# Kernel optimization log

Measured on AMD Instinct MI355X. Metric: run time of the kernel, lower is better.

## Reference

```python
import jax, jax.numpy as jnp
import numpy as np

E, M, K, N = 32, 1024, 512, 512

def setup_inputs() -> dict:
    key = jax.random.key(0)
    k1, k2, k3 = jax.random.split(key, 3)
    A = jax.random.normal(k1, (E, M, K), dtype=jnp.float32)
    B = jax.random.normal(k2, (E, N, K), dtype=jnp.float32)
    expert_num_tokens = jax.random.randint(k3, (E,), 0, M + 1, dtype=jnp.int32)
    return {"A": A, "B": B, "expert_num_tokens": expert_num_tokens}

def reference(A, B, expert_num_tokens):
    # Per-expert GEMM: C[e] = A[e] @ B[e].T  -> [E, M, N]
    C = jnp.einsum('emk,enk->emn', A, B)
    # Rows m >= expert_num_tokens[e] are never computed/stored by the kernel;
    # zero them in the reference output.
    row_valid = jnp.arange(A.shape[1])[None, :] < expert_num_tokens[:, None]  # [E, M]
    return jnp.where(row_valid[:, :, None], C, jnp.zeros((), C.dtype))
```

## Files before the change

kernel.cpp:

```cpp
#include <hip/hip_runtime.h>
#include <hip/hip_bf16.h>

#define NE 32
#define MM 1024
#define KK 512
#define NN 512
#define BM 128
#define BN 128
#define BK 32
#define LDST (BK + 8)

typedef __attribute__((ext_vector_type(8))) short bf16x8;
typedef __attribute__((ext_vector_type(4))) short shortx4;
typedef __attribute__((ext_vector_type(4))) float floatx4;

__device__ __forceinline__ short f2bf(float f) {
  union { __hip_bfloat16 b; short s; } u;
  u.b = __float2bfloat16(f);
  return u.s;
}

extern "C" __global__ __launch_bounds__(256, 2)
void expert_gemm(const float* __restrict__ A, const float* __restrict__ B,
                 const int* __restrict__ cnts, float* __restrict__ C)
{
  const int bid = blockIdx.x;
  const int e   = bid >> 5;
  const int rem = bid & 31;
  const int mt  = rem >> 2;
  const int nt  = rem & 3;
  const int m0  = mt * BM;
  const int n0  = nt * BN;
  const int cnt = cnts[e];
  const int tid = threadIdx.x;

  float* Ce = C + ((size_t)e * MM + m0) * NN + n0;

  if (m0 >= cnt) {
    float4 z = make_float4(0.f, 0.f, 0.f, 0.f);
#pragma unroll
    for (int i = 0; i < 16; ++i) {
      int idx = i * 256 + tid;
      int r = idx >> 5;
      int c = (idx & 31) << 2;
      *(float4*)(Ce + (size_t)r * NN + c) = z;
    }
    return;
  }

  const float* Ae = A + ((size_t)e * MM + m0) * KK;
  const float* Be = B + ((size_t)e * NN + n0) * KK;

  __shared__ __align__(16) short lA[BM * LDST];
  __shared__ __align__(16) short lB[BN * LDST];

  const int wave = tid >> 6;
  const int lane = tid & 63;
  const int wm = (wave >> 1) * 64;
  const int wn = (wave & 1) * 64;
  const int fr = lane & 15;
  const int kh = lane >> 4;

  const int srow = tid >> 3;
  const int scol = (tid & 7) << 2;

  floatx4 acc[4][4] = {};

  float4 ra[4], rbv[4];
#pragma unroll
  for (int p = 0; p < 4; ++p) {
    ra[p]  = *(const float4*)(Ae + (size_t)(srow + p * 32) * KK + scol);
    rbv[p] = *(const float4*)(Be + (size_t)(srow + p * 32) * KK + scol);
  }

  for (int kt = 0; kt < KK; kt += BK) {
    __syncthreads();
#pragma unroll
    for (int p = 0; p < 4; ++p) {
      shortx4 va = { f2bf(ra[p].x),  f2bf(ra[p].y),  f2bf(ra[p].z),  f2bf(ra[p].w)  };
      shortx4 vb = { f2bf(rbv[p].x), f2bf(rbv[p].y), f2bf(rbv[p].z), f2bf(rbv[p].w) };
      *(shortx4*)(lA + (srow + p * 32) * LDST + scol) = va;
      *(shortx4*)(lB + (srow + p * 32) * LDST + scol) = vb;
    }
    __syncthreads();

    if (kt + BK < KK) {
#pragma unroll
      for (int p = 0; p < 4; ++p) {
        ra[p]  = *(const float4*)(Ae + (size_t)(srow + p * 32) * KK + kt + BK + scol);
        rbv[p] = *(const float4*)(Be + (size_t)(srow + p * 32) * KK + kt + BK + scol);
      }
    }

    bf16x8 af[4], bfv[4];
#pragma unroll
    for (int i = 0; i < 4; ++i) {
      af[i]  = *(bf16x8*)(lA + (wm + i * 16 + fr) * LDST + kh * 8);
      bfv[i] = *(bf16x8*)(lB + (wn + i * 16 + fr) * LDST + kh * 8);
    }
#pragma unroll
    for (int i = 0; i < 4; ++i)
#pragma unroll
      for (int j = 0; j < 4; ++j)
        acc[i][j] = __builtin_amdgcn_mfma_f32_16x16x32_bf16(af[i], bfv[j], acc[i][j], 0, 0, 0);
  }

  const int rb_ = (lane >> 4) * 4;
#pragma unroll
  for (int i = 0; i < 4; ++i) {
#pragma unroll
    for (int r = 0; r < 4; ++r) {
      int row = wm + i * 16 + rb_ + r;
      bool valid = (m0 + row) < cnt;
#pragma unroll
      for (int j = 0; j < 4; ++j) {
        int col = wn + j * 16 + fr;
        Ce[(size_t)row * NN + col] = valid ? acc[i][j][r] : 0.0f;
      }
    }
  }
}

extern "C" void kernel_launch(void* const* d_in, const int* in_sizes, int n_in,
                              void* d_out, int out_size, void* d_ws, size_t ws_size,
                              hipStream_t stream) {
  const float* A    = (const float*)d_in[0];
  const float* B    = (const float*)d_in[1];
  const int*   cnts = (const int*)d_in[2];
  float*       C    = (float*)d_out;

  dim3 grid(NE * (MM / BM) * (NN / BN));
  dim3 block(256);
  hipLaunchKernelGGL(expert_gemm, grid, block, 0, stream, A, B, cnts, C);
}
```

Measured before the change: 173.0 us.

## Use persistent blocks with an atomic work queue over valid tiles

Adds a single-thread prepass kernel that builds a compacted list of valid GEMM tiles followed by zero-fill row-tile items. The GEMM launches 512 persistent blocks that pull items from the list through an atomic counter, so idle blocks for empty tiles no longer occupy the grid and load balances across CUs. The serial prepass and the per-item atomics and barriers add latency, and it relies on the workspace being large enough.

```diff
diff --git a/kernel.cpp b/kernel.cpp
--- a/kernel.cpp
+++ b/kernel.cpp
@@ -9,6 +9,8 @@
 #define BN 128
 #define BK 32
 #define LDST (BK + 8)
+#define NMT (MM / BM)
+#define NNT (NN / BN)
 
 typedef __attribute__((ext_vector_type(8))) short bf16x8;
 typedef __attribute__((ext_vector_type(4))) short shortx4;
@@ -20,102 +22,128 @@
   return u.s;
 }
 
+extern "C" __global__ void prepass(const int* __restrict__ cnts,
+                                   unsigned int* __restrict__ q) {
+  if (threadIdx.x == 0 && blockIdx.x == 0) {
+    int w = 2;
+    for (int e = 0; e < NE; ++e) {
+      int vt = (cnts[e] + BM - 1) / BM;
+      for (int mt = 0; mt < vt; ++mt)
+        for (int nt = 0; nt < NNT; ++nt)
+          q[w++] = ((unsigned)e << 16) | ((unsigned)mt << 8) | (unsigned)nt;
+    }
+    for (int e = 0; e < NE; ++e) {
+      int vt = (cnts[e] + BM - 1) / BM;
+      for (int mt = vt; mt < NMT; ++mt)
+        q[w++] = 0x80000000u | ((unsigned)e << 16) | ((unsigned)mt << 8);
+    }
+    q[1] = (unsigned)(w - 2);
+    q[0] = 0u;
+  }
+}
+
 extern "C" __global__ __launch_bounds__(256, 2)
 void expert_gemm(const float* __restrict__ A, const float* __restrict__ B,
-                 const int* __restrict__ cnts, float* __restrict__ C)
+                 const int* __restrict__ cnts, float* __restrict__ C,
+                 unsigned int* __restrict__ q)
 {
-  const int bid = blockIdx.x;
-  const int e   = bid >> 5;
-  const int rem = bid & 31;
-  const int mt  = rem >> 2;
-  const int nt  = rem & 3;
-  const int m0  = mt * BM;
-  const int n0  = nt * BN;
-  const int cnt = cnts[e];
-  const int tid = threadIdx.x;
-
-  float* Ce = C + ((size_t)e * MM + m0) * NN + n0;
-
-  if (m0 >= cnt) {
-    float4 z = make_float4(0.f, 0.f, 0.f, 0.f);
-#pragma unroll
-    for (int i = 0; i < 16; ++i) {
-      int idx = i * 256 + tid;
-      int r = idx >> 5;
-      int c = (idx & 31) << 2;
-      *(float4*)(Ce + (size_t)r * NN + c) = z;
-    }
-    return;
-  }
-
-  const float* Ae = A + ((size_t)e * MM + m0) * KK;
-  const float* Be = B + ((size_t)e * NN + n0) * KK;
-
   __shared__ __align__(16) short lA[BM * LDST];
   __shared__ __align__(16) short lB[BN * LDST];
+  __shared__ unsigned int item_s;
 
+  const int tid  = threadIdx.x;
   const int wave = tid >> 6;
   const int lane = tid & 63;
   const int wm = (wave >> 1) * 64;
   const int wn = (wave & 1) * 64;
   const int fr = lane & 15;
   const int kh = lane >> 4;
-
   const int srow = tid >> 3;
   const int scol = (tid & 7) << 2;
+  const unsigned total = q[1];
 
-  floatx4 acc[4][4] = {};
+  for (;;) {
+    __syncthreads();
+    if (tid == 0) item_s = atomicAdd(&q[0], 1u);
+    __syncthreads();
+    unsigned idx = item_s;
+    if (idx >= total) break;
+    unsigned it = q[2 + idx];
+    int e  = (it >> 16) & 0xFF;
+    int mt = (it >> 8) & 0xFF;
 
-  float4 ra[4], rbv[4];
+    if (it & 0x80000000u) {
+      float* Ce = C + ((size_t)e * MM + mt * BM) * NN;
+      float4 z = make_float4(0.f, 0.f, 0.f, 0.f);
 #pragma unroll
-  for (int p = 0; p < 4; ++p) {
-    ra[p]  = *(const float4*)(Ae + (size_t)(srow + p * 32) * KK + scol);
-    rbv[p] = *(const float4*)(Be + (size_t)(srow + p * 32) * KK + scol);
-  }
+      for (int i = 0; i < 64; ++i) {
+        int fidx = i * 256 + tid;
+        int r = fidx >> 7;
+        int c = (fidx & 127) << 2;
+        *(float4*)(Ce + (size_t)r * NN + c) = z;
+      }
+      continue;
+    }
 
-  for (int kt = 0; kt < KK; kt += BK) {
-    __syncthreads();
+    int nt = it & 0xFF;
+    int m0 = mt * BM, n0 = nt * BN;
+    int cnt = cnts[e];
+    const float* Ae = A + ((size_t)e * MM + m0) * KK;
+    const float* Be = B + ((size_t)e * NN + n0) * KK;
+    float* Ce = C + ((size_t)e * MM + m0) * NN + n0;
+
+    floatx4 acc[4][4] = {};
+    float4 ra[4], rbv[4];
 #pragma unroll
     for (int p = 0; p < 4; ++p) {
-      shortx4 va = { f2bf(ra[p].x),  f2bf(ra[p].y),  f2bf(ra[p].z),  f2bf(ra[p].w)  };
-      shortx4 vb = { f2bf(rbv[p].x), f2bf(rbv[p].y), f2bf(rbv[p].z), f2bf(rbv[p].w) };
-      *(shortx4*)(lA + (srow + p * 32) * LDST + scol) = va;
-      *(shortx4*)(lB + (srow + p * 32) * LDST + scol) = vb;
+      ra[p]  = *(const float4*)(Ae + (size_t)(srow + p * 32) * KK + scol);
+      rbv[p] = *(const float4*)(Be + (size_t)(srow + p * 32) * KK + scol);
     }
-    __syncthreads();
 
-    if (kt + BK < KK) {
+    for (int kt = 0; kt < KK; kt += BK) {
+      __syncthreads();
 #pragma unroll
       for (int p = 0; p < 4; ++p) {
-        ra[p]  = *(const float4*)(Ae + (size_t)(srow + p * 32) * KK + kt + BK + scol);
-        rbv[p] = *(const float4*)(Be + (size_t)(srow + p * 32) * KK + kt + BK + scol);
+        shortx4 va = { f2bf(ra[p].x),  f2bf(ra[p].y),  f2bf(ra[p].z),  f2bf(ra[p].w)  };
+        shortx4 vb = { f2bf(rbv[p].x), f2bf(rbv[p].y), f2bf(rbv[p].z), f2bf(rbv[p].w) };
+        *(shortx4*)(lA + (srow + p * 32) * LDST + scol) = va;
+        *(shortx4*)(lB + (srow + p * 32) * LDST + scol) = vb;
       }
+      __syncthreads();
+
+      if (kt + BK < KK) {
+#pragma unroll
+        for (int p = 0; p < 4; ++p) {
+          ra[p]  = *(const float4*)(Ae + (size_t)(srow + p * 32) * KK + kt + BK + scol);
+          rbv[p] = *(const float4*)(Be + (size_t)(srow + p * 32) * KK + kt + BK + scol);
+        }
+      }
+
+      bf16x8 af[4], bfv[4];
+#pragma unroll
+      for (int i = 0; i < 4; ++i) {
+        af[i]  = *(bf16x8*)(lA + (wm + i * 16 + fr) * LDST + kh * 8);
+        bfv[i] = *(bf16x8*)(lB + (wn + i * 16 + fr) * LDST + kh * 8);
+      }
+#pragma unroll
+      for (int i = 0; i < 4; ++i)
+#pragma unroll
+        for (int j = 0; j < 4; ++j)
+          acc[i][j] = __builtin_amdgcn_mfma_f32_16x16x32_bf16(af[i], bfv[j], acc[i][j], 0, 0, 0);
     }
 
-    bf16x8 af[4], bfv[4];
+    const int rb_ = (lane >> 4) * 4;
 #pragma unroll
     for (int i = 0; i < 4; ++i) {
-      af[i]  = *(bf16x8*)(lA + (wm + i * 16 + fr) * LDST + kh * 8);
-      bfv[i] = *(bf16x8*)(lB + (wn + i * 16 + fr) * LDST + kh * 8);
-    }
 #pragma unroll
-    for (int i = 0; i < 4; ++i)
+      for (int r = 0; r < 4; ++r) {
+        int row = wm + i * 16 + rb_ + r;
+        bool valid = (m0 + row) < cnt;
 #pragma unroll
-      for (int j = 0; j < 4; ++j)
-        acc[i][j] = __builtin_amdgcn_mfma_f32_16x16x32_bf16(af[i], bfv[j], acc[i][j], 0, 0, 0);
-  }
-
-  const int rb_ = (lane >> 4) * 4;
-#pragma unroll
-  for (int i = 0; i < 4; ++i) {
-#pragma unroll
-    for (int r = 0; r < 4; ++r) {
-      int row = wm + i * 16 + rb_ + r;
-      bool valid = (m0 + row) < cnt;
-#pragma unroll
-      for (int j = 0; j < 4; ++j) {
-        int col = wn + j * 16 + fr;
-        Ce[(size_t)row * NN + col] = valid ? acc[i][j][r] : 0.0f;
+        for (int j = 0; j < 4; ++j) {
+          int col = wn + j * 16 + fr;
+          Ce[(size_t)row * NN + col] = valid ? acc[i][j][r] : 0.0f;
+        }
       }
     }
   }
@@ -128,8 +156,8 @@
   const float* B    = (const float*)d_in[1];
   const int*   cnts = (const int*)d_in[2];
   float*       C    = (float*)d_out;
+  unsigned int* q   = (unsigned int*)d_ws;
 
-  dim3 grid(NE * (MM / BM) * (NN / BN));
-  dim3 block(256);
-  hipLaunchKernelGGL(expert_gemm, grid, block, 0, stream, A, B, cnts, C);
+  hipLaunchKernelGGL(prepass, dim3(1), dim3(64), 0, stream, cnts, q);
+  hipLaunchKernelGGL(expert_gemm, dim3(512), dim3(256), 0, stream, A, B, cnts, C, q);
 }
```

After: 183.2 us. 1.06x slower.

## Compact grid to valid tiles, XOR-swizzle LDS, drop register prefetch

Applied to the files above, without the earlier changes.

Each block now scans the per-expert token counts and maps itself onto a compacted list. Valid GEMM tiles come first; after them come full-row zero-fill blocks that clear 128x512 strips. This gets rid of the scattered early-exit blocks and balances the work across the grid. The LDS padding is replaced by an XOR swizzle with 16-byte bf16x8 stores, and launch bounds rise to 4 blocks per SM. In exchange the global-load prefetch that overlapped with compute is removed, and every block pays a serial 32-iteration scan over the counts.

```diff
diff --git a/kernel.cpp b/kernel.cpp
--- a/kernel.cpp
+++ b/kernel.cpp
@@ -8,10 +8,8 @@
 #define BM 128
 #define BN 128
 #define BK 32
-#define LDST (BK + 8)
 
 typedef __attribute__((ext_vector_type(8))) short bf16x8;
-typedef __attribute__((ext_vector_type(4))) short shortx4;
 typedef __attribute__((ext_vector_type(4))) float floatx4;
 
 __device__ __forceinline__ short f2bf(float f) {
@@ -20,89 +18,100 @@
   return u.s;
 }
 
-extern "C" __global__ __launch_bounds__(256, 2)
+extern "C" __global__ __launch_bounds__(256, 4)
 void expert_gemm(const float* __restrict__ A, const float* __restrict__ B,
                  const int* __restrict__ cnts, float* __restrict__ C)
 {
-  const int bid = blockIdx.x;
-  const int e   = bid >> 5;
-  const int rem = bid & 31;
-  const int mt  = rem >> 2;
-  const int nt  = rem & 3;
-  const int m0  = mt * BM;
-  const int n0  = nt * BN;
-  const int cnt = cnts[e];
+  const int b   = blockIdx.x;
   const int tid = threadIdx.x;
 
-  float* Ce = C + ((size_t)e * MM + m0) * NN + n0;
-
-  if (m0 >= cnt) {
-    float4 z = make_float4(0.f, 0.f, 0.f, 0.f);
+  int e = -1, mt = 0, nt = 0;
+  int acc = 0;
+#pragma unroll 1
+  for (int i = 0; i < NE; ++i) {
+    int vt = (cnts[i] + BM - 1) >> 7;
+    int c4 = vt << 2;
+    if (e < 0 && b < acc + c4) { int r = b - acc; e = i; mt = r >> 2; nt = r & 3; }
+    acc += c4;
+  }
+  if (e < 0) {
+    int z = b - acc, a2 = 0;
+#pragma unroll 1
+    for (int i = 0; i < NE; ++i) {
+      int vt = (cnts[i] + BM - 1) >> 7;
+      int c = 8 - vt;
+      if (e < 0 && z < a2 + c) { e = i; mt = vt + (z - a2); }
+      a2 += c;
+    }
+    if (e < 0) return;
+    float* Ce = C + ((size_t)e * MM + mt * BM) * NN;
+    float4 zf = make_float4(0.f, 0.f, 0.f, 0.f);
 #pragma unroll
-    for (int i = 0; i < 16; ++i) {
-      int idx = i * 256 + tid;
-      int r = idx >> 5;
-      int c = (idx & 31) << 2;
-      *(float4*)(Ce + (size_t)r * NN + c) = z;
+    for (int i = 0; i < 64; ++i) {
+      int fidx = i * 256 + tid;
+      int r = fidx >> 7, c = (fidx & 127) << 2;
+      *(float4*)(Ce + (size_t)r * NN + c) = zf;
     }
     return;
   }
 
+  const int m0 = mt * BM, n0 = nt * BN;
+  const int cnt = cnts[e];
   const float* Ae = A + ((size_t)e * MM + m0) * KK;
   const float* Be = B + ((size_t)e * NN + n0) * KK;
+  float* Ce = C + ((size_t)e * MM + m0) * NN + n0;
 
-  __shared__ __align__(16) short lA[BM * LDST];
-  __shared__ __align__(16) short lB[BN * LDST];
+  __shared__ __align__(16) short lA[BM * BK];
+  __shared__ __align__(16) short lB[BN * BK];
 
-  const int wave = tid >> 6;
-  const int lane = tid & 63;
-  const int wm = (wave >> 1) * 64;
-  const int wn = (wave & 1) * 64;
-  const int fr = lane & 15;
-  const int kh = lane >> 4;
+  const int wave = tid >> 6, lane = tid & 63;
+  const int wm = (wave >> 1) * 64, wn = (wave & 1) * 64;
+  const int fr = lane & 15, kh = lane >> 4;
 
-  const int srow = tid >> 3;
-  const int scol = (tid & 7) << 2;
+  const int srow = tid >> 2;
+  const int su   = tid & 3;
 
-  floatx4 acc[4][4] = {};
-
-  float4 ra[4], rbv[4];
-#pragma unroll
-  for (int p = 0; p < 4; ++p) {
-    ra[p]  = *(const float4*)(Ae + (size_t)(srow + p * 32) * KK + scol);
-    rbv[p] = *(const float4*)(Be + (size_t)(srow + p * 32) * KK + scol);
-  }
+  floatx4 acc4[4][4] = {};
 
   for (int kt = 0; kt < KK; kt += BK) {
+    float4 a0[2], a1[2], b0[2], b1[2];
+#pragma unroll
+    for (int p = 0; p < 2; ++p) {
+      int row = srow + (p << 6);
+      int col = kt + (su << 3);
+      a0[p] = *(const float4*)(Ae + (size_t)row * KK + col);
+      a1[p] = *(const float4*)(Ae + (size_t)row * KK + col + 4);
+      b0[p] = *(const float4*)(Be + (size_t)row * KK + col);
+      b1[p] = *(const float4*)(Be + (size_t)row * KK + col + 4);
+    }
+
     __syncthreads();
 #pragma unroll
-    for (int p = 0; p < 4; ++p) {
-      shortx4 va = { f2bf(ra[p].x),  f2bf(ra[p].y),  f2bf(ra[p].z),  f2bf(ra[p].w)  };
-      shortx4 vb = { f2bf(rbv[p].x), f2bf(rbv[p].y), f2bf(rbv[p].z), f2bf(rbv[p].w) };
-      *(shortx4*)(lA + (srow + p * 32) * LDST + scol) = va;
-      *(shortx4*)(lB + (srow + p * 32) * LDST + scol) = vb;
+    for (int p = 0; p < 2; ++p) {
+      int row = srow + (p << 6);
+      int unit = (row << 2) + (su ^ (row & 3));
+      bf16x8 va = { f2bf(a0[p].x), f2bf(a0[p].y), f2bf(a0[p].z), f2bf(a0[p].w),
+                    f2bf(a1[p].x), f2bf(a1[p].y), f2bf(a1[p].z), f2bf(a1[p].w) };
+      bf16x8 vb = { f2bf(b0[p].x), f2bf(b0[p].y), f2bf(b0[p].z), f2bf(b0[p].w),
+                    f2bf(b1[p].x), f2bf(b1[p].y), f2bf(b1[p].z), f2bf(b1[p].w) };
+      *(bf16x8*)(lA + (unit << 3)) = va;
+      *(bf16x8*)(lB + (unit << 3)) = vb;
     }
     __syncthreads();
-
-    if (kt + BK < KK) {
-#pragma unroll
-      for (int p = 0; p < 4; ++p) {
-        ra[p]  = *(const float4*)(Ae + (size_t)(srow + p * 32) * KK + kt + BK + scol);
-        rbv[p] = *(const float4*)(Be + (size_t)(srow + p * 32) * KK + kt + BK + scol);
-      }
-    }
 
     bf16x8 af[4], bfv[4];
 #pragma unroll
     for (int i = 0; i < 4; ++i) {
-      af[i]  = *(bf16x8*)(lA + (wm + i * 16 + fr) * LDST + kh * 8);
-      bfv[i] = *(bf16x8*)(lB + (wn + i * 16 + fr) * LDST + kh * 8);
+      int rA = wm + (i << 4) + fr;
+      af[i]  = *(const bf16x8*)(lA + ((((rA << 2) + (kh ^ (rA & 3)))) << 3));
+      int rB = wn + (i << 4) + fr;
+      bfv[i] = *(const bf16x8*)(lB + ((((rB << 2) + (kh ^ (rB & 3)))) << 3));
     }
 #pragma unroll
     for (int i = 0; i < 4; ++i)
 #pragma unroll
       for (int j = 0; j < 4; ++j)
-        acc[i][j] = __builtin_amdgcn_mfma_f32_16x16x32_bf16(af[i], bfv[j], acc[i][j], 0, 0, 0);
+        acc4[i][j] = __builtin_amdgcn_mfma_f32_16x16x32_bf16(af[i], bfv[j], acc4[i][j], 0, 0, 0);
   }
 
   const int rb_ = (lane >> 4) * 4;
@@ -115,7 +124,7 @@
 #pragma unroll
       for (int j = 0; j < 4; ++j) {
         int col = wn + j * 16 + fr;
-        Ce[(size_t)row * NN + col] = valid ? acc[i][j][r] : 0.0f;
+        Ce[(size_t)row * NN + col] = valid ? acc4[i][j][r] : 0.0f;
       }
     }
   }
@@ -129,7 +138,5 @@
   const int*   cnts = (const int*)d_in[2];
   float*       C    = (float*)d_out;
 
-  dim3 grid(NE * (MM / BM) * (NN / BN));
-  dim3 block(256);
-  hipLaunchKernelGGL(expert_gemm, grid, block, 0, stream, A, B, cnts, C);
+  hipLaunchKernelGGL(expert_gemm, dim3(1024), dim3(256), 0, stream, A, B, cnts, C);
 }
```

After: 159.4 us. 7.9% less time.
